# Optimization experiments

Measured on AMD Instinct MI355X. Metric: run time of the kernel, lower is better.

The kernel has to match this reference:

```python
import jax, jax.numpy as jnp
import numpy as np
import math

# dims: batch, seq_len, d_model, heads, head_dim
B, L, DM, H, DH = 1, 4096, 1024, 16, 64
BS, W, MAXD, DFF = 64, 16, 256, 4096  # block_size, band width (blocks), max rel distance, ffn dim
NB = L // BS


def _static_layout():
    # Static block-sparse causal band layout: tgt block n attends to src blocks [n-W+1 .. n].
    # Mirrors construct_blocksparse_rel_ids: rel = tgt_pos - src_pos, pos ids start at 1
    # (0 reserved for padding), clamp rel<-1 -> -1, rel>max_distance -> max_distance, then +1.
    n = np.arange(NB)[:, None, None, None]
    w = np.arange(W)[None, :, None, None]
    i = np.arange(BS)[None, None, :, None]
    j = np.arange(BS)[None, None, None, :]
    src_blk = n - (W - 1) + w
    # valid: block exists; diagonal block (w==W-1) is causal within-block (j<=i)
    valid = (src_blk >= 0) & ((w < W - 1) | (j <= i))
    tgt_pos = n * BS + i + 1
    src_pos = np.clip(src_blk, 0, None) * BS + j + 1
    rel = np.clip(tgt_pos - src_pos, -1, MAXD) + 1
    rel = np.where(valid, rel, 0)  # masked positions get rel id 0 (as in masked_fill_)
    src_idx = np.clip(np.arange(NB)[:, None] - (W - 1) + np.arange(W)[None, :], 0, None)
    return jnp.asarray(rel), jnp.asarray(valid), jnp.asarray(src_idx)

REL_IDS, VALID, SRC_IDX = _static_layout()  # [NB,W,BS,BS], [NB,W,BS,BS], [NB,W]


def _ln(x, g, b):
    m = x.mean(-1, keepdims=True)
    v = ((x - m) ** 2).mean(-1, keepdims=True)
    return (x - m) * jax.lax.rsqrt(v + 1e-5) * g + b


def setup_inputs() -> dict:
    key = jax.random.key(0)
    ks = jax.random.split(key, 10)
    p = lambda k, shape: jax.random.normal(k, shape, jnp.float32) * 0.02
    return dict(
        x=jax.random.normal(ks[0], (B, L, DM), jnp.float32),
        Wq=p(ks[1], (DM, DM)), Wk=p(ks[2], (DM, DM)), Wv=p(ks[3], (DM, DM)),
        Wo=p(ks[4], (DM, DM)),
        rel_emb=p(ks[5], (MAXD + 2, H)),  # per-head relative position bias table
        ln1_g=jnp.ones((DM,), jnp.float32), ln1_b=jnp.zeros((DM,), jnp.float32),
        ln2_g=jnp.ones((DM,), jnp.float32), ln2_b=jnp.zeros((DM,), jnp.float32),
        W1=p(ks[6], (DM, DFF)), b1=jnp.zeros((DFF,), jnp.float32),
        W2=p(ks[7], (DFF, DM)), b2=jnp.zeros((DM,), jnp.float32),
    )


def reference(x, Wq, Wk, Wv, Wo, rel_emb, ln1_g, ln1_b, ln2_g, ln2_b, W1, b1, W2, b2):
    h = _ln(x, ln1_g, ln1_b)

    def heads(Wt):
        return (h @ Wt).reshape(B, NB, BS, H, DH).transpose(0, 3, 1, 2, 4)  # [B,H,NB,BS,DH]

    q, k, v = heads(Wq), heads(Wk), heads(Wv)
    k_band = k[:, :, SRC_IDX]  # gather nonzero src blocks -> [B,H,NB,W,BS,DH]
    v_band = v[:, :, SRC_IDX]
    scores = jnp.einsum('bhnid,bhnwjd->bhniwj', q, k_band) / math.sqrt(DH)
    # relative position bias, per block pair and head
    bias = rel_emb[REL_IDS].transpose(4, 0, 2, 1, 3)  # [H,NB,BS,W,BS]
    scores = scores + bias[None]
    mask = VALID.transpose(0, 2, 1, 3)  # [NB,BS,W,BS]
    scores = jnp.where(mask, scores, jnp.float32(-1e30))
    p = jax.nn.softmax(scores.reshape(B, H, NB, BS, W * BS), axis=-1)
    p = p.reshape(B, H, NB, BS, W, BS)
    o = jnp.einsum('bhniwj,bhnwjd->bhnid', p, v_band)
    o = o.transpose(0, 2, 3, 1, 4).reshape(B, L, DM) @ Wo
    x = x + o
    h2 = _ln(x, ln2_g, ln2_b)
    x = x + (jax.nn.gelu(h2 @ W1 + b1) @ W2 + b2)
    return x
```

## Files before the change

kernel.cpp:

```cpp
#include <hip/hip_runtime.h>
#include <math.h>

typedef __bf16 bf16x8 __attribute__((ext_vector_type(8)));
typedef short  s16x4  __attribute__((ext_vector_type(4)));
typedef float  f32x4  __attribute__((ext_vector_type(4)));
typedef short  s16x8  __attribute__((ext_vector_type(8)));

__device__ __forceinline__ unsigned short f2bf(float f) {
    unsigned int u = __float_as_uint(f);
    u += 0x7fffu + ((u >> 16) & 1u);
    return (unsigned short)(u >> 16);
}

__device__ __forceinline__ unsigned cvt_pk_bf16(float a, float b) {
    unsigned r;
    asm volatile("v_cvt_pk_bf16_f32 %0, %1, %2" : "=v"(r) : "v"(a), "v"(b));
    return r;
}

__device__ __forceinline__ f32x4 mfma16(s16x4 a, s16x4 b, f32x4 c) {
#if __has_builtin(__builtin_amdgcn_mfma_f32_16x16x16bf16_1k)
    return __builtin_amdgcn_mfma_f32_16x16x16bf16_1k(a, b, c, 0, 0, 0);
#else
    asm volatile("s_nop 3\n\t"
                 "v_mfma_f32_16x16x16_bf16 %0, %1, %2, %0\n\t"
                 "s_nop 7\n\t"
                 "s_nop 7"
                 : "+v"(c) : "v"(a), "v"(b));
    return c;
#endif
}

__device__ __forceinline__ float gelu_tanh(float x) {
    float x3 = x * x * x;
    float t = tanhf(0.7978845608028654f * (x + 0.044715f * x3));
    return 0.5f * x * (1.0f + t);
}

__global__ __launch_bounds__(256) void tcvt_kernel(const float* __restrict__ in,
                                                   unsigned short* __restrict__ out,
                                                   int K, int N) {
    __shared__ float tile[32][33];
    int tx = threadIdx.x, ty = threadIdx.y;
    int k0 = blockIdx.y * 32, n0 = blockIdx.x * 32;
#pragma unroll
    for (int s = 0; s < 4; ++s)
        tile[ty + s * 8][tx] = in[(size_t)(k0 + ty + s * 8) * N + n0 + tx];
    __syncthreads();
#pragma unroll
    for (int s = 0; s < 4; ++s)
        out[(size_t)(n0 + ty + s * 8) * K + k0 + tx] = f2bf(tile[tx][ty + s * 8]);
}

__global__ __launch_bounds__(256) void ln_kernel(const float* __restrict__ x,
                                                 const float* __restrict__ g,
                                                 const float* __restrict__ b,
                                                 unsigned short* __restrict__ out) {
    int row = blockIdx.x;
    int tid = threadIdx.x;
    float4 v = ((const float4*)(x + (size_t)row * 1024))[tid];
    float s  = v.x + v.y + v.z + v.w;
    float ss = v.x * v.x + v.y * v.y + v.z * v.z + v.w * v.w;
#pragma unroll
    for (int o = 32; o > 0; o >>= 1) { s += __shfl_down(s, o); ss += __shfl_down(ss, o); }
    __shared__ float red[8];
    if ((tid & 63) == 0) { red[(tid >> 6) * 2] = s; red[(tid >> 6) * 2 + 1] = ss; }
    __syncthreads();
    s  = red[0] + red[2] + red[4] + red[6];
    ss = red[1] + red[3] + red[5] + red[7];
    float mean = s * (1.0f / 1024.0f);
    float var  = ss * (1.0f / 1024.0f) - mean * mean;
    float rs   = rsqrtf(var + 1e-5f);
    float4 gv = ((const float4*)g)[tid];
    float4 bv = ((const float4*)b)[tid];
    ushort4 o4;
    o4.x = f2bf((v.x - mean) * rs * gv.x + bv.x);
    o4.y = f2bf((v.y - mean) * rs * gv.y + bv.y);
    o4.z = f2bf((v.z - mean) * rs * gv.z + bv.z);
    o4.w = f2bf((v.w - mean) * rs * gv.w + bv.w);
    ((ushort4*)(out + (size_t)row * 1024))[tid] = o4;
}

__global__ __launch_bounds__(256) void tvt_kernel(const unsigned short* __restrict__ in,
                                                  unsigned short* __restrict__ out) {
    __shared__ unsigned short tile[64][72];
    int t = threadIdx.x;
    int l0 = blockIdx.x * 64, c0 = blockIdx.y * 64;
    int tr = t >> 3, tc = (t & 7) * 8;
#pragma unroll
    for (int s = 0; s < 2; ++s) {
        int r = tr + s * 32;
        s16x8 v = *(const s16x8*)(in + (size_t)(l0 + r) * 3072 + 2048 + c0 + tc);
        *(s16x8*)(&tile[r][tc]) = v;
    }
    __syncthreads();
#pragma unroll
    for (int s = 0; s < 2; ++s) {
        int c = tr + s * 32;
        s16x8 w;
#pragma unroll
        for (int e = 0; e < 8; ++e) w[e] = (short)tile[tc + e][c];
        *(s16x8*)(out + (size_t)(c0 + c) * 4096 + l0 + tc) = w;
    }
}

__device__ __forceinline__ void stage8(const unsigned short* __restrict__ src_row0, int ld,
                                       unsigned short* ldsdst, int lane) {
    const int r8 = lane >> 3;
    const int c  = (lane & 7) ^ r8;
    const unsigned short* src = src_row0 + (size_t)r8 * ld + c * 8;
    __builtin_amdgcn_global_load_lds((const __attribute__((address_space(1))) void*)src,
                                     (__attribute__((address_space(3))) void*)ldsdst, 16, 0, 0);
}

__device__ __forceinline__ void stage64(const unsigned short* __restrict__ mat, int ld,
                                        int grow0, int kcol,
                                        unsigned short* lds_tile, int q, int wave, int lane) {
    const int l8 = lane >> 3;
    const int sc = ((lane & 7) ^ l8) << 3;
    const unsigned short* src = mat + (size_t)(grow0 + q * 64 + wave * 8 + l8) * ld + kcol + sc;
    unsigned short* dst = lds_tile + ((q * 64 + wave * 8) << 6);
    __builtin_amdgcn_global_load_lds((const __attribute__((address_space(1))) void*)src,
                                     (__attribute__((address_space(3))) void*)dst, 16, 0, 0);
}

__device__ __forceinline__ bf16x8 ldfrag(const unsigned short* tile, int row, int chunk) {
    return *(const bf16x8*)(tile + (row << 6) + (((chunk ^ row) & 7) << 3));
}

__device__ __forceinline__ s16x4 ldfrag64(const unsigned short* tile, int row, int ch16, int half) {
    return *(const s16x4*)(tile + (row << 6) + (((ch16 ^ row) & 7) << 3) + (half << 2));
}

template <int EPI>
__global__ __launch_bounds__(512, 2) void gemm256_kernel(
        const unsigned short* __restrict__ A, int lda,
        const unsigned short* __restrict__ Bt, int ldb,
        void* __restrict__ Cv, const float* __restrict__ bias,
        int ldc, int NT, int gm, int gn, unsigned long long slab_stride) {
    extern __shared__ unsigned short lds[];
    unsigned short* sA = lds;
    unsigned short* sB = lds + 2 * 256 * 64;

    const int tid  = threadIdx.x;
    const int wave = tid >> 6, lane = tid & 63;
    const int wr = wave >> 2, wc = wave & 3;
    const int lg = lane >> 4, l15 = lane & 15;

    const int nwg = gridDim.x;
    const int bid = blockIdx.x;
    const int q8 = nwg >> 3, r8 = nwg & 7;
    const int xcd = bid & 7, loc = bid >> 3;
    const int swz = (xcd < r8 ? xcd * (q8 + 1) : r8 * (q8 + 1) + (xcd - r8) * q8) + loc;
    const int split = swz / (gm * gn);
    const int rem   = swz % (gm * gn);
    const int brow = (rem / gn) << 8;
    const int bcol = (rem % gn) << 8;
    const int kbase = split * (NT << 6);

    f32x4 acc[8][4] = {};

#define STAGE_A(tt, q_, pbuf) stage64(A, lda, brow, kbase + ((tt) << 6), sA + (pbuf) * 16384, (q_), wave, lane)
#define STAGE_B(tt, q_, pbuf) stage64(Bt, ldb, bcol, kbase + ((tt) << 6), sB + (pbuf) * 16384, (q_), wave, lane)

    STAGE_A(0, 0, 0); STAGE_A(0, 1, 0); STAGE_A(0, 2, 0); STAGE_A(0, 3, 0);
    STAGE_B(0, 0, 0); STAGE_B(0, 1, 0); STAGE_B(0, 2, 0); STAGE_B(0, 3, 0);
    STAGE_A(1, 0, 1); STAGE_A(1, 1, 1); STAGE_A(1, 2, 1); STAGE_A(1, 3, 1);
    STAGE_B(1, 0, 1); STAGE_B(1, 1, 1);
    asm volatile("s_waitcnt vmcnt(6)" ::: "memory");
    __builtin_amdgcn_s_barrier();

    for (int t = 0; t < NT; ++t) {
        const int p = t & 1;
        const unsigned short* tA = sA + p * 16384;
        const unsigned short* tB = sB + p * 16384;
        bf16x8 a0[4][2], a1[4][2], b0[2][2], b1[2][2];

#pragma unroll
        for (int im = 0; im < 4; ++im)
#pragma unroll
            for (int kk = 0; kk < 2; ++kk)
                a0[im][kk] = ldfrag(tA, wr * 128 + im * 16 + l15, lg + kk * 4);
#pragma unroll
        for (int in = 0; in < 2; ++in)
#pragma unroll
            for (int kk = 0; kk < 2; ++kk)
                b0[in][kk] = ldfrag(tB, wc * 64 + in * 16 + l15, lg + kk * 4);
        if (t + 1 < NT) { STAGE_B(t + 1, 2, p ^ 1); STAGE_B(t + 1, 3, p ^ 1); }
        __builtin_amdgcn_s_barrier();
        asm volatile("s_waitcnt lgkmcnt(0)" ::: "memory");
        __builtin_amdgcn_sched_barrier(0);
        __builtin_amdgcn_s_setprio(1);
#pragma unroll
        for (int kk = 0; kk < 2; ++kk)
#pragma unroll
            for (int im = 0; im < 4; ++im)
#pragma unroll
                for (int in = 0; in < 2; ++in)
                    acc[im][in] = __builtin_amdgcn_mfma_f32_16x16x32_bf16(a0[im][kk], b0[in][kk], acc[im][in], 0, 0, 0);
        __builtin_amdgcn_s_setprio(0);
        __builtin_amdgcn_s_barrier();

#pragma unroll
        for (int im = 0; im < 4; ++im)
#pragma unroll
            for (int kk = 0; kk < 2; ++kk)
                a1[im][kk] = ldfrag(tA, wr * 128 + 64 + im * 16 + l15, lg + kk * 4);
        if (t + 2 < NT) { STAGE_A(t + 2, 0, p); STAGE_A(t + 2, 2, p); }
        __builtin_amdgcn_s_barrier();
        asm volatile("s_waitcnt lgkmcnt(0)" ::: "memory");
        __builtin_amdgcn_sched_barrier(0);
        __builtin_amdgcn_s_setprio(1);
#pragma unroll
        for (int kk = 0; kk < 2; ++kk)
#pragma unroll
            for (int im = 0; im < 4; ++im)
#pragma unroll
                for (int in = 0; in < 2; ++in)
                    acc[4 + im][in] = __builtin_amdgcn_mfma_f32_16x16x32_bf16(a1[im][kk], b0[in][kk], acc[4 + im][in], 0, 0, 0);
        __builtin_amdgcn_s_setprio(0);
        __builtin_amdgcn_s_barrier();

#pragma unroll
        for (int in = 0; in < 2; ++in)
#pragma unroll
            for (int kk = 0; kk < 2; ++kk)
                b1[in][kk] = ldfrag(tB, wc * 64 + 32 + in * 16 + l15, lg + kk * 4);
        if (t + 2 < NT) { STAGE_A(t + 2, 1, p); STAGE_A(t + 2, 3, p); }
        __builtin_amdgcn_s_barrier();
        asm volatile("s_waitcnt lgkmcnt(0)" ::: "memory");
        __builtin_amdgcn_sched_barrier(0);
        __builtin_amdgcn_s_setprio(1);
#pragma unroll
        for (int kk = 0; kk < 2; ++kk)
#pragma unroll
            for (int im = 0; im < 4; ++im)
#pragma unroll
                for (int in = 0; in < 2; ++in)
                    acc[4 + im][2 + in] = __builtin_amdgcn_mfma_f32_16x16x32_bf16(a1[im][kk], b1[in][kk], acc[4 + im][2 + in], 0, 0, 0);
        __builtin_amdgcn_s_setprio(0);
        __builtin_amdgcn_s_barrier();

        if (t + 2 < NT) { STAGE_B(t + 2, 0, p); STAGE_B(t + 2, 1, p); }
        __builtin_amdgcn_s_barrier();
        asm volatile("s_waitcnt lgkmcnt(0)" ::: "memory");
        __builtin_amdgcn_sched_barrier(0);
        __builtin_amdgcn_s_setprio(1);
#pragma unroll
        for (int kk = 0; kk < 2; ++kk)
#pragma unroll
            for (int im = 0; im < 4; ++im)
#pragma unroll
                for (int in = 0; in < 2; ++in)
                    acc[im][2 + in] = __builtin_amdgcn_mfma_f32_16x16x32_bf16(a0[im][kk], b1[in][kk], acc[im][2 + in], 0, 0, 0);
        __builtin_amdgcn_s_setprio(0);
        if (t + 2 < NT) asm volatile("s_waitcnt vmcnt(6)" ::: "memory");
        else            asm volatile("s_waitcnt vmcnt(0)" ::: "memory");
        __builtin_amdgcn_s_barrier();
    }
#undef STAGE_A
#undef STAGE_B

#pragma unroll
    for (int mi = 0; mi < 8; ++mi)
#pragma unroll
        for (int ni = 0; ni < 4; ++ni)
#pragma unroll
            for (int rr = 0; rr < 4; ++rr) {
                int row = brow + wr * 128 + mi * 16 + lg * 4 + rr;
                int col = bcol + wc * 64 + ni * 16 + l15;
                float v = acc[mi][ni][rr];
                if (EPI == 0) {
                    ((unsigned short*)Cv)[(size_t)row * ldc + col] = f2bf(v);
                } else if (EPI == 2) {
                    v += bias[col];
                    ((unsigned short*)Cv)[(size_t)row * ldc + col] = f2bf(gelu_tanh(v));
                } else {
                    ((unsigned short*)Cv)[slab_stride * split + (size_t)row * ldc + col] = f2bf(v);
                }
            }
}

template <int HB>
__global__ __launch_bounds__(256) void reduce4_kernel(const unsigned short* __restrict__ part,
                                                      const float* __restrict__ bias,
                                                      const float* __restrict__ resid,
                                                      float* __restrict__ out) {
    int i4 = blockIdx.x * 256 + threadIdx.x;
    float4 r  = ((const float4*)resid)[i4];
    float s0 = r.x, s1 = r.y, s2 = r.z, s3 = r.w;
    if (HB) {
        float4 bb = ((const float4*)bias)[i4 & 255];
        s0 += bb.x; s1 += bb.y; s2 += bb.z; s3 += bb.w;
    }
#pragma unroll
    for (int s = 0; s < 4; ++s) {
        ushort4 u = ((const ushort4*)(part + (size_t)s * 4194304))[i4];
        s0 += __uint_as_float((unsigned)u.x << 16);
        s1 += __uint_as_float((unsigned)u.y << 16);
        s2 += __uint_as_float((unsigned)u.z << 16);
        s3 += __uint_as_float((unsigned)u.w << 16);
    }
    float4 o; o.x = s0; o.y = s1; o.z = s2; o.w = s3;
    ((float4*)out)[i4] = o;
}

__global__ __launch_bounds__(512, 4) void attn3_kernel(const unsigned short* __restrict__ qkv,
                                                       const unsigned short* __restrict__ vt,
                                                       const float* __restrict__ rel_emb,
                                                       unsigned short* __restrict__ outp) {
    const int lid   = blockIdx.y * gridDim.x + blockIdx.x;
    const int rid   = (lid & 7) * 64 + (lid >> 3);
    const int h     = rid >> 5;
    const int strip = rid & 31;
    const int n0    = strip * 2;

    const int tid  = threadIdx.x;
    const int wv   = tid >> 6;
    const int lane = tid & 63;
    const int qb   = wv >> 2;
    const int lg   = lane >> 4;
    const int l15  = lane & 15;
    const int iq   = (wv & 3) * 16 + l15;
    const int q0   = n0 * 64 + wv * 16;

    __shared__ __align__(16) unsigned short sK[2][4096];
    __shared__ __align__(16) unsigned short sV[2][4096];
    __shared__ float sRelF[258];

    bf16x8 qf[2];
    {
        const unsigned short* qrow = qkv + (size_t)(q0 + l15) * 3072 + h * 64 + lg * 8;
        qf[0] = *(const bf16x8*)(qrow);
        qf[1] = *(const bf16x8*)(qrow + 32);
    }

    for (int i = tid; i < 258; i += 512) sRelF[i] = rel_emb[i * 16 + h];
    const float relC = rel_emb[257 * 16 + h];

    const int tlo = (n0 >= 15) ? 0 : (15 - n0);
    {
        const int src = n0 - 15 + tlo;
        stage8(qkv + (size_t)(src * 64 + wv * 8) * 3072 + 1024 + h * 64, 3072, &sK[0][wv * 8 * 64], lane);
        stage8(vt + (size_t)(h * 64 + wv * 8) * 4096 + src * 64, 4096, &sV[0][wv * 8 * 64], lane);
    }
    asm volatile("s_waitcnt lgkmcnt(0)" ::: "memory");
    __builtin_amdgcn_s_barrier();

    f32x4 oacc[4] = {};
    float mrow = -3e38f, lrow = 0.f;

    for (int t = tlo; t <= 16; ++t) {
        const int cur = (t - tlo) & 1;
        if (t < 16) {
            const int src = n0 - 15 + (t + 1);
            stage8(qkv + (size_t)(src * 64 + wv * 8) * 3072 + 1024 + h * 64, 3072, &sK[cur ^ 1][wv * 8 * 64], lane);
            stage8(vt + (size_t)(h * 64 + wv * 8) * 4096 + src * 64, 4096, &sV[cur ^ 1][wv * 8 * 64], lane);
            asm volatile("s_waitcnt vmcnt(2)" ::: "memory");
        } else {
            asm volatile("s_waitcnt vmcnt(0)" ::: "memory");
        }
        __builtin_amdgcn_s_barrier();

        const bool act = (t >= qb) && (t - qb <= 15);
        if (act) {
            const unsigned short* tK = &sK[cur][0];
            const unsigned short* tV = &sV[cur][0];
            const int woff = 15 + qb - t;

            f32x4 st[4] = {};
            __builtin_amdgcn_s_setprio(1);
#pragma unroll
            for (int jt = 0; jt < 4; ++jt) {
                bf16x8 kf0 = ldfrag(tK, jt * 16 + l15, lg);
                bf16x8 kf1 = ldfrag(tK, jt * 16 + l15, lg + 4);
                st[jt] = __builtin_amdgcn_mfma_f32_16x16x32_bf16(kf0, qf[0], st[jt], 0, 0, 0);
                st[jt] = __builtin_amdgcn_mfma_f32_16x16x32_bf16(kf1, qf[1], st[jt], 0, 0, 0);
            }
            __builtin_amdgcn_s_setprio(0);

            float pm = -3e38f;
            if (woff >= 5) {
#pragma unroll
                for (int jt = 0; jt < 4; ++jt)
#pragma unroll
                    for (int rr = 0; rr < 4; ++rr) {
                        float v = st[jt][rr] * 0.125f + relC;
                        st[jt][rr] = v;
                        pm = fmaxf(pm, v);
                    }
            } else if (woff > 0) {
#pragma unroll
                for (int jt = 0; jt < 4; ++jt)
#pragma unroll
                    for (int rr = 0; rr < 4; ++rr) {
                        int j = jt * 16 + lg * 4 + rr;
                        int relid = min(woff * 64 + iq - j, 256) + 1;
                        float v = st[jt][rr] * 0.125f + sRelF[relid];
                        st[jt][rr] = v;
                        pm = fmaxf(pm, v);
                    }
            } else {
#pragma unroll
                for (int jt = 0; jt < 4; ++jt)
#pragma unroll
                    for (int rr = 0; rr < 4; ++rr) {
                        int j = jt * 16 + lg * 4 + rr;
                        float v = (j <= iq) ? (st[jt][rr] * 0.125f + sRelF[iq - j + 1]) : -1e30f;
                        st[jt][rr] = v;
                        pm = fmaxf(pm, v);
                    }
            }
            pm = fmaxf(pm, __shfl_xor(pm, 16));
            pm = fmaxf(pm, __shfl_xor(pm, 32));
            float mn  = fmaxf(mrow, pm);
            float scl = __expf(mrow - mn);
            mrow = mn;

            float rs = 0.f;
            unsigned pk0[4], pk1[4];
#pragma unroll
            for (int jt = 0; jt < 4; ++jt) {
                float p0 = __expf(st[jt][0] - mn);
                float p1 = __expf(st[jt][1] - mn);
                float p2 = __expf(st[jt][2] - mn);
                float p3 = __expf(st[jt][3] - mn);
                rs += (p0 + p1) + (p2 + p3);
                pk0[jt] = cvt_pk_bf16(p0, p1);
                pk1[jt] = cvt_pk_bf16(p2, p3);
            }
            rs += __shfl_xor(rs, 16);
            rs += __shfl_xor(rs, 32);
            lrow = lrow * scl + rs;
#pragma unroll
            for (int dt = 0; dt < 4; ++dt)
#pragma unroll
                for (int rr = 0; rr < 4; ++rr)
                    oacc[dt][rr] *= scl;

            __builtin_amdgcn_s_setprio(1);
#pragma unroll
            for (int ks = 0; ks < 4; ++ks) {
                union { unsigned u[2]; s16x4 v; } pu;
                pu.u[0] = pk0[ks]; pu.u[1] = pk1[ks];
#pragma unroll
                for (int dt = 0; dt < 4; ++dt) {
                    s16x4 vf = ldfrag64(tV, dt * 16 + l15, 2 * ks + (lg >> 1), lg & 1);
                    oacc[dt] = mfma16(vf, pu.v, oacc[dt]);
                }
            }
            __builtin_amdgcn_s_setprio(0);
        }
        __builtin_amdgcn_s_barrier();
    }

    float inv = 1.0f / lrow;
    unsigned short* sO = &sK[0][0] + wv * 1024;
#pragma unroll
    for (int dt = 0; dt < 4; ++dt)
#pragma unroll
        for (int c = 0; c < 2; ++c) {
            unsigned pr = cvt_pk_bf16(oacc[dt][2 * c] * inv, oacc[dt][2 * c + 1] * inv);
            int d  = dt * 16 + lg * 4 + 2 * c;
            int off = (l15 << 6) + ((((d >> 3) ^ (l15 & 7)) & 7) << 3) + (d & 7);
            *(unsigned*)(sO + off) = pr;
        }
#pragma unroll
    for (int c2 = 0; c2 < 2; ++c2) {
        int ch = lg + 4 * c2;
        bf16x8 ov = ldfrag(sO, l15, ch);
        *(s16x8*)(outp + (size_t)(q0 + l15) * 1024 + h * 64 + ch * 8) = *(const s16x8*)&ov;
    }
}

extern "C" void kernel_launch(void* const* d_in, const int* in_sizes, int n_in,
                              void* d_out, int out_size, void* d_ws, size_t ws_size,
                              hipStream_t stream) {
    const float* x    = (const float*)d_in[0];
    const float* Wq   = (const float*)d_in[1];
    const float* Wk   = (const float*)d_in[2];
    const float* Wv   = (const float*)d_in[3];
    const float* Wo   = (const float*)d_in[4];
    const float* rel  = (const float*)d_in[5];
    const float* ln1g = (const float*)d_in[6];
    const float* ln1b = (const float*)d_in[7];
    const float* ln2g = (const float*)d_in[8];
    const float* ln2b = (const float*)d_in[9];
    const float* W1   = (const float*)d_in[10];
    const float* b1   = (const float*)d_in[11];
    const float* W2   = (const float*)d_in[12];
    const float* b2   = (const float*)d_in[13];

    char* ws = (char*)d_ws;
    unsigned short* wqkvT  = (unsigned short*)(ws + 0);
    unsigned short* woT    = (unsigned short*)(ws + 6291456);
    unsigned short* attnb  = (unsigned short*)(ws + 8388608);
    unsigned short* w1T    = (unsigned short*)(ws + 16777216);
    unsigned short* hbuf   = (unsigned short*)(ws + 25165824);
    unsigned short* w2T    = (unsigned short*)(ws + 33554432);
    float*          x2     = (float*)(ws + 41943040);
    unsigned short* qkv    = (unsigned short*)(ws + 58720256);
    unsigned short* vt     = (unsigned short*)(ws + 83886080);
    unsigned short* wopart = (unsigned short*)(ws + 58720256);
    unsigned short* gbuf   = (unsigned short*)(ws + 58720256);
    unsigned short* part   = (unsigned short*)(ws + 0);

    const int smem = 131072;
    hipFuncSetAttribute((const void*)gemm256_kernel<0>, hipFuncAttributeMaxDynamicSharedMemorySize, smem);
    hipFuncSetAttribute((const void*)gemm256_kernel<2>, hipFuncAttributeMaxDynamicSharedMemorySize, smem);
    hipFuncSetAttribute((const void*)gemm256_kernel<4>, hipFuncAttributeMaxDynamicSharedMemorySize, smem);

    dim3 tb(32, 8);
    tcvt_kernel<<<dim3(32, 32), tb, 0, stream>>>(Wq, wqkvT, 1024, 1024);
    tcvt_kernel<<<dim3(32, 32), tb, 0, stream>>>(Wk, wqkvT + 1048576, 1024, 1024);
    tcvt_kernel<<<dim3(32, 32), tb, 0, stream>>>(Wv, wqkvT + 2097152, 1024, 1024);
    tcvt_kernel<<<dim3(32, 32), tb, 0, stream>>>(Wo, woT, 1024, 1024);
    tcvt_kernel<<<dim3(128, 32), tb, 0, stream>>>(W1, w1T, 1024, 4096);
    tcvt_kernel<<<dim3(32, 128), tb, 0, stream>>>(W2, w2T, 4096, 1024);

    ln_kernel<<<4096, 256, 0, stream>>>(x, ln1g, ln1b, hbuf);

    gemm256_kernel<0><<<192, 512, smem, stream>>>(hbuf, 1024, wqkvT, 1024, qkv,
                                                  nullptr, 3072, 16, 16, 12, 0ULL);

    tvt_kernel<<<dim3(64, 16), 256, 0, stream>>>(qkv, vt);

    attn3_kernel<<<dim3(32, 16), 512, 0, stream>>>(qkv, vt, rel, attnb);

    gemm256_kernel<4><<<256, 512, smem, stream>>>(attnb, 1024, woT, 1024, wopart,
                                                  nullptr, 1024, 4, 16, 4, 4194304ULL);
    reduce4_kernel<0><<<4096, 256, 0, stream>>>(wopart, nullptr, x, x2);

    ln_kernel<<<4096, 256, 0, stream>>>(x2, ln2g, ln2b, hbuf);

    gemm256_kernel<2><<<256, 512, smem, stream>>>(hbuf, 1024, w1T, 1024, gbuf,
                                                  b1, 4096, 16, 16, 16, 0ULL);

    gemm256_kernel<4><<<256, 512, smem, stream>>>(gbuf, 4096, w2T, 4096, part,
                                                  nullptr, 1024, 16, 16, 4, 4194304ULL);

    reduce4_kernel<1><<<4096, 256, 0, stream>>>(part, b2, x2, (float*)d_out);
}
```

Before: 246.6 us.

## Fuse reduce+LN2, batch weight converts, reshape attention blocks, band-swizzle GEMM tiles

Merges the Wo split-K reduction with the second layernorm so x2 is not re-read. Merges four weight transpose-convert launches into one 3D-grid launch. Restructures attention so each 256-thread block handles one query block instead of two, which removes the inactive-wave iterations of the paired-strip schedule. Remaps GEMM tile order into bands of four column tiles for better L2 reuse. The changes add more attention blocks with less K/V sharing per block.

```diff
diff --git a/kernel.cpp b/kernel.cpp
--- a/kernel.cpp
+++ b/kernel.cpp
@@ -35,6 +35,26 @@
     float x3 = x * x * x;
     float t = tanhf(0.7978845608028654f * (x + 0.044715f * x3));
     return 0.5f * x * (1.0f + t);
+}
+
+__global__ __launch_bounds__(256) void tcvt4_kernel(const float* __restrict__ p0,
+                                                    const float* __restrict__ p1,
+                                                    const float* __restrict__ p2,
+                                                    const float* __restrict__ p3,
+                                                    unsigned short* __restrict__ out) {
+    __shared__ float tile[32][33];
+    int z = blockIdx.z;
+    const float* in = (z == 0) ? p0 : (z == 1) ? p1 : (z == 2) ? p2 : p3;
+    unsigned short* o = out + (size_t)z * 1048576;
+    int tx = threadIdx.x, ty = threadIdx.y;
+    int k0 = blockIdx.y * 32, n0 = blockIdx.x * 32;
+#pragma unroll
+    for (int s = 0; s < 4; ++s)
+        tile[ty + s * 8][tx] = in[(size_t)(k0 + ty + s * 8) * 1024 + n0 + tx];
+    __syncthreads();
+#pragma unroll
+    for (int s = 0; s < 4; ++s)
+        o[(size_t)(n0 + ty + s * 8) * 1024 + k0 + tx] = f2bf(tile[tx][ty + s * 8]);
 }
 
 __global__ __launch_bounds__(256) void tcvt_kernel(const float* __restrict__ in,
@@ -81,6 +101,50 @@
     ((ushort4*)(out + (size_t)row * 1024))[tid] = o4;
 }
 
+__global__ __launch_bounds__(256) void reduceln_kernel(const unsigned short* __restrict__ part,
+                                                       const float* __restrict__ xin,
+                                                       const float* __restrict__ g,
+                                                       const float* __restrict__ b,
+                                                       float* __restrict__ x2,
+                                                       unsigned short* __restrict__ outbf) {
+    int row = blockIdx.x;
+    int tid = threadIdx.x;
+    int i4  = row * 256 + tid;
+    float4 r = ((const float4*)xin)[i4];
+    float v0 = r.x, v1 = r.y, v2 = r.z, v3 = r.w;
+#pragma unroll
+    for (int sl = 0; sl < 4; ++sl) {
+        ushort4 u = ((const ushort4*)(part + (size_t)sl * 4194304))[i4];
+        v0 += __uint_as_float((unsigned)u.x << 16);
+        v1 += __uint_as_float((unsigned)u.y << 16);
+        v2 += __uint_as_float((unsigned)u.z << 16);
+        v3 += __uint_as_float((unsigned)u.w << 16);
+    }
+    float4 o; o.x = v0; o.y = v1; o.z = v2; o.w = v3;
+    ((float4*)x2)[i4] = o;
+
+    float s  = v0 + v1 + v2 + v3;
+    float ss = v0 * v0 + v1 * v1 + v2 * v2 + v3 * v3;
+#pragma unroll
+    for (int off = 32; off > 0; off >>= 1) { s += __shfl_down(s, off); ss += __shfl_down(ss, off); }
+    __shared__ float red[8];
+    if ((tid & 63) == 0) { red[(tid >> 6) * 2] = s; red[(tid >> 6) * 2 + 1] = ss; }
+    __syncthreads();
+    s  = red[0] + red[2] + red[4] + red[6];
+    ss = red[1] + red[3] + red[5] + red[7];
+    float mean = s * (1.0f / 1024.0f);
+    float var  = ss * (1.0f / 1024.0f) - mean * mean;
+    float rs   = rsqrtf(var + 1e-5f);
+    float4 gv = ((const float4*)g)[tid];
+    float4 bv = ((const float4*)b)[tid];
+    ushort4 o4;
+    o4.x = f2bf((v0 - mean) * rs * gv.x + bv.x);
+    o4.y = f2bf((v1 - mean) * rs * gv.y + bv.y);
+    o4.z = f2bf((v2 - mean) * rs * gv.z + bv.z);
+    o4.w = f2bf((v3 - mean) * rs * gv.w + bv.w);
+    ((ushort4*)(outbf + (size_t)row * 1024))[tid] = o4;
+}
+
 __global__ __launch_bounds__(256) void tvt_kernel(const unsigned short* __restrict__ in,
                                                   unsigned short* __restrict__ out) {
     __shared__ unsigned short tile[64][72];
@@ -154,8 +218,10 @@
     const int swz = (xcd < r8 ? xcd * (q8 + 1) : r8 * (q8 + 1) + (xcd - r8) * q8) + loc;
     const int split = swz / (gm * gn);
     const int rem   = swz % (gm * gn);
-    const int brow = (rem / gn) << 8;
-    const int bcol = (rem % gn) << 8;
+    const int band = rem / (gm * 4);
+    const int r2   = rem % (gm * 4);
+    const int brow = (r2 >> 2) << 8;
+    const int bcol = (band * 4 + (r2 & 3)) << 8;
     const int kbase = split * (NT << 6);
 
     f32x4 acc[8][4] = {};
@@ -281,18 +347,14 @@
             }
 }
 
-template <int HB>
 __global__ __launch_bounds__(256) void reduce4_kernel(const unsigned short* __restrict__ part,
                                                       const float* __restrict__ bias,
                                                       const float* __restrict__ resid,
                                                       float* __restrict__ out) {
     int i4 = blockIdx.x * 256 + threadIdx.x;
     float4 r  = ((const float4*)resid)[i4];
-    float s0 = r.x, s1 = r.y, s2 = r.z, s3 = r.w;
-    if (HB) {
-        float4 bb = ((const float4*)bias)[i4 & 255];
-        s0 += bb.x; s1 += bb.y; s2 += bb.z; s3 += bb.w;
-    }
+    float4 bb = ((const float4*)bias)[i4 & 255];
+    float s0 = r.x + bb.x, s1 = r.y + bb.y, s2 = r.z + bb.z, s3 = r.w + bb.w;
 #pragma unroll
     for (int s = 0; s < 4; ++s) {
         ushort4 u = ((const ushort4*)(part + (size_t)s * 4194304))[i4];
@@ -305,24 +367,22 @@
     ((float4*)out)[i4] = o;
 }
 
-__global__ __launch_bounds__(512, 4) void attn3_kernel(const unsigned short* __restrict__ qkv,
+__global__ __launch_bounds__(256, 4) void attn4_kernel(const unsigned short* __restrict__ qkv,
                                                        const unsigned short* __restrict__ vt,
                                                        const float* __restrict__ rel_emb,
                                                        unsigned short* __restrict__ outp) {
-    const int lid   = blockIdx.y * gridDim.x + blockIdx.x;
-    const int rid   = (lid & 7) * 64 + (lid >> 3);
-    const int h     = rid >> 5;
-    const int strip = rid & 31;
-    const int n0    = strip * 2;
+    const int lid = blockIdx.y * gridDim.x + blockIdx.x;
+    const int rid = (lid & 7) * 128 + (lid >> 3);
+    const int h   = rid >> 6;
+    const int n   = rid & 63;
 
     const int tid  = threadIdx.x;
     const int wv   = tid >> 6;
     const int lane = tid & 63;
-    const int qb   = wv >> 2;
     const int lg   = lane >> 4;
     const int l15  = lane & 15;
-    const int iq   = (wv & 3) * 16 + l15;
-    const int q0   = n0 * 64 + wv * 16;
+    const int iq   = wv * 16 + l15;
+    const int q0   = n * 64 + wv * 16;
 
     __shared__ __align__(16) unsigned short sK[2][4096];
     __shared__ __align__(16) unsigned short sV[2][4096];
@@ -335,14 +395,18 @@
         qf[1] = *(const bf16x8*)(qrow + 32);
     }
 
-    for (int i = tid; i < 258; i += 512) sRelF[i] = rel_emb[i * 16 + h];
+    for (int i = tid; i < 258; i += 256) sRelF[i] = rel_emb[i * 16 + h];
     const float relC = rel_emb[257 * 16 + h];
 
-    const int tlo = (n0 >= 15) ? 0 : (15 - n0);
+    const int tlo = (n >= 15) ? 0 : (15 - n);
     {
-        const int src = n0 - 15 + tlo;
-        stage8(qkv + (size_t)(src * 64 + wv * 8) * 3072 + 1024 + h * 64, 3072, &sK[0][wv * 8 * 64], lane);
-        stage8(vt + (size_t)(h * 64 + wv * 8) * 4096 + src * 64, 4096, &sV[0][wv * 8 * 64], lane);
+        const int src = n - 15 + tlo;
+#pragma unroll
+        for (int s = 0; s < 2; ++s) {
+            int r0 = wv * 16 + s * 8;
+            stage8(qkv + (size_t)(src * 64 + r0) * 3072 + 1024 + h * 64, 3072, &sK[0][r0 * 64], lane);
+            stage8(vt + (size_t)(h * 64 + r0) * 4096 + src * 64, 4096, &sV[0][r0 * 64], lane);
+        }
     }
     asm volatile("s_waitcnt lgkmcnt(0)" ::: "memory");
     __builtin_amdgcn_s_barrier();
@@ -350,107 +414,108 @@
     f32x4 oacc[4] = {};
     float mrow = -3e38f, lrow = 0.f;
 
-    for (int t = tlo; t <= 16; ++t) {
+    for (int t = tlo; t < 16; ++t) {
         const int cur = (t - tlo) & 1;
-        if (t < 16) {
-            const int src = n0 - 15 + (t + 1);
-            stage8(qkv + (size_t)(src * 64 + wv * 8) * 3072 + 1024 + h * 64, 3072, &sK[cur ^ 1][wv * 8 * 64], lane);
-            stage8(vt + (size_t)(h * 64 + wv * 8) * 4096 + src * 64, 4096, &sV[cur ^ 1][wv * 8 * 64], lane);
-            asm volatile("s_waitcnt vmcnt(2)" ::: "memory");
+        if (t < 15) {
+            const int src = n - 15 + (t + 1);
+#pragma unroll
+            for (int s = 0; s < 2; ++s) {
+                int r0 = wv * 16 + s * 8;
+                stage8(qkv + (size_t)(src * 64 + r0) * 3072 + 1024 + h * 64, 3072, &sK[cur ^ 1][r0 * 64], lane);
+                stage8(vt + (size_t)(h * 64 + r0) * 4096 + src * 64, 4096, &sV[cur ^ 1][r0 * 64], lane);
+            }
+            asm volatile("s_waitcnt vmcnt(4)" ::: "memory");
         } else {
             asm volatile("s_waitcnt vmcnt(0)" ::: "memory");
         }
         __builtin_amdgcn_s_barrier();
 
-        const bool act = (t >= qb) && (t - qb <= 15);
-        if (act) {
-            const unsigned short* tK = &sK[cur][0];
-            const unsigned short* tV = &sV[cur][0];
-            const int woff = 15 + qb - t;
-
-            f32x4 st[4] = {};
-            __builtin_amdgcn_s_setprio(1);
-#pragma unroll
-            for (int jt = 0; jt < 4; ++jt) {
-                bf16x8 kf0 = ldfrag(tK, jt * 16 + l15, lg);
-                bf16x8 kf1 = ldfrag(tK, jt * 16 + l15, lg + 4);
-                st[jt] = __builtin_amdgcn_mfma_f32_16x16x32_bf16(kf0, qf[0], st[jt], 0, 0, 0);
-                st[jt] = __builtin_amdgcn_mfma_f32_16x16x32_bf16(kf1, qf[1], st[jt], 0, 0, 0);
+        const unsigned short* tK = &sK[cur][0];
+        const unsigned short* tV = &sV[cur][0];
+        const int woff = 15 - t;
+
+        f32x4 st[4] = {};
+        __builtin_amdgcn_s_setprio(1);
+#pragma unroll
+        for (int jt = 0; jt < 4; ++jt) {
+            bf16x8 kf0 = ldfrag(tK, jt * 16 + l15, lg);
+            bf16x8 kf1 = ldfrag(tK, jt * 16 + l15, lg + 4);
+            st[jt] = __builtin_amdgcn_mfma_f32_16x16x32_bf16(kf0, qf[0], st[jt], 0, 0, 0);
+            st[jt] = __builtin_amdgcn_mfma_f32_16x16x32_bf16(kf1, qf[1], st[jt], 0, 0, 0);
+        }
+        __builtin_amdgcn_s_setprio(0);
+
+        float pm = -3e38f;
+        if (woff >= 5) {
+#pragma unroll
+            for (int jt = 0; jt < 4; ++jt)
+#pragma unroll
+                for (int rr = 0; rr < 4; ++rr) {
+                    float v = st[jt][rr] * 0.125f + relC;
+                    st[jt][rr] = v;
+                    pm = fmaxf(pm, v);
+                }
+        } else if (woff > 0) {
+#pragma unroll
+            for (int jt = 0; jt < 4; ++jt)
+#pragma unroll
+                for (int rr = 0; rr < 4; ++rr) {
+                    int j = jt * 16 + lg * 4 + rr;
+                    int relid = min(woff * 64 + iq - j, 256) + 1;
+                    float v = st[jt][rr] * 0.125f + sRelF[relid];
+                    st[jt][rr] = v;
+                    pm = fmaxf(pm, v);
+                }
+        } else {
+#pragma unroll
+            for (int jt = 0; jt < 4; ++jt)
+#pragma unroll
+                for (int rr = 0; rr < 4; ++rr) {
+                    int j = jt * 16 + lg * 4 + rr;
+                    float v = (j <= iq) ? (st[jt][rr] * 0.125f + sRelF[iq - j + 1]) : -1e30f;
+                    st[jt][rr] = v;
+                    pm = fmaxf(pm, v);
+                }
+        }
+        pm = fmaxf(pm, __shfl_xor(pm, 16));
+        pm = fmaxf(pm, __shfl_xor(pm, 32));
+        float mn  = fmaxf(mrow, pm);
+        float scl = __expf(mrow - mn);
+        mrow = mn;
+
+        float rs = 0.f;
+        unsigned pk0[4], pk1[4];
+#pragma unroll
+        for (int jt = 0; jt < 4; ++jt) {
+            float p0 = __expf(st[jt][0] - mn);
+            float p1 = __expf(st[jt][1] - mn);
+            float p2 = __expf(st[jt][2] - mn);
+            float p3 = __expf(st[jt][3] - mn);
+            rs += (p0 + p1) + (p2 + p3);
+            pk0[jt] = cvt_pk_bf16(p0, p1);
+            pk1[jt] = cvt_pk_bf16(p2, p3);
+        }
+        rs += __shfl_xor(rs, 16);
+        rs += __shfl_xor(rs, 32);
+        lrow = lrow * scl + rs;
+#pragma unroll
+        for (int dt = 0; dt < 4; ++dt)
+#pragma unroll
+            for (int rr = 0; rr < 4; ++rr)
+                oacc[dt][rr] *= scl;
+
+        __builtin_amdgcn_s_setprio(1);
+#pragma unroll
+        for (int ks = 0; ks < 4; ++ks) {
+            union { unsigned u[2]; s16x4 v; } pu;
+            pu.u[0] = pk0[ks]; pu.u[1] = pk1[ks];
+#pragma unroll
+            for (int dt = 0; dt < 4; ++dt) {
+                s16x4 vf = ldfrag64(tV, dt * 16 + l15, 2 * ks + (lg >> 1), lg & 1);
+                oacc[dt] = mfma16(vf, pu.v, oacc[dt]);
             }
-            __builtin_amdgcn_s_setprio(0);
-
-            float pm = -3e38f;
-            if (woff >= 5) {
-#pragma unroll
-                for (int jt = 0; jt < 4; ++jt)
-#pragma unroll
-                    for (int rr = 0; rr < 4; ++rr) {
-                        float v = st[jt][rr] * 0.125f + relC;
-                        st[jt][rr] = v;
-                        pm = fmaxf(pm, v);
-                    }
-            } else if (woff > 0) {
-#pragma unroll
-                for (int jt = 0; jt < 4; ++jt)
-#pragma unroll
-                    for (int rr = 0; rr < 4; ++rr) {
-                        int j = jt * 16 + lg * 4 + rr;
-                        int relid = min(woff * 64 + iq - j, 256) + 1;
-                        float v = st[jt][rr] * 0.125f + sRelF[relid];
-                        st[jt][rr] = v;
-                        pm = fmaxf(pm, v);
-                    }
-            } else {
-#pragma unroll
-                for (int jt = 0; jt < 4; ++jt)
-#pragma unroll
-                    for (int rr = 0; rr < 4; ++rr) {
-                        int j = jt * 16 + lg * 4 + rr;
-                        float v = (j <= iq) ? (st[jt][rr] * 0.125f + sRelF[iq - j + 1]) : -1e30f;
-                        st[jt][rr] = v;
-                        pm = fmaxf(pm, v);
-                    }
-            }
-            pm = fmaxf(pm, __shfl_xor(pm, 16));
-            pm = fmaxf(pm, __shfl_xor(pm, 32));
-            float mn  = fmaxf(mrow, pm);
-            float scl = __expf(mrow - mn);
-            mrow = mn;
-
-            float rs = 0.f;
-            unsigned pk0[4], pk1[4];
-#pragma unroll
-            for (int jt = 0; jt < 4; ++jt) {
-                float p0 = __expf(st[jt][0] - mn);
-                float p1 = __expf(st[jt][1] - mn);
-                float p2 = __expf(st[jt][2] - mn);
-                float p3 = __expf(st[jt][3] - mn);
-                rs += (p0 + p1) + (p2 + p3);
-                pk0[jt] = cvt_pk_bf16(p0, p1);
-                pk1[jt] = cvt_pk_bf16(p2, p3);
-            }
-            rs += __shfl_xor(rs, 16);
-            rs += __shfl_xor(rs, 32);
-            lrow = lrow * scl + rs;
-#pragma unroll
-            for (int dt = 0; dt < 4; ++dt)
-#pragma unroll
-                for (int rr = 0; rr < 4; ++rr)
-                    oacc[dt][rr] *= scl;
-
-            __builtin_amdgcn_s_setprio(1);
-#pragma unroll
-            for (int ks = 0; ks < 4; ++ks) {
-                union { unsigned u[2]; s16x4 v; } pu;
-                pu.u[0] = pk0[ks]; pu.u[1] = pk1[ks];
-#pragma unroll
-                for (int dt = 0; dt < 4; ++dt) {
-                    s16x4 vf = ldfrag64(tV, dt * 16 + l15, 2 * ks + (lg >> 1), lg & 1);
-                    oacc[dt] = mfma16(vf, pu.v, oacc[dt]);
-                }
-            }
-            __builtin_amdgcn_s_setprio(0);
         }
+        __builtin_amdgcn_s_setprio(0);
         __builtin_amdgcn_s_barrier();
     }
 
@@ -493,7 +558,7 @@
 
     char* ws = (char*)d_ws;
     unsigned short* wqkvT  = (unsigned short*)(ws + 0);
-    unsigned short* woT    = (unsigned short*)(ws + 6291456);
+    unsigned short* woT    = wqkvT + 3145728;
     unsigned short* attnb  = (unsigned short*)(ws + 8388608);
     unsigned short* w1T    = (unsigned short*)(ws + 16777216);
     unsigned short* hbuf   = (unsigned short*)(ws + 25165824);
@@ -511,10 +576,7 @@
     hipFuncSetAttribute((const void*)gemm256_kernel<4>, hipFuncAttributeMaxDynamicSharedMemorySize, smem);
 
     dim3 tb(32, 8);
-    tcvt_kernel<<<dim3(32, 32), tb, 0, stream>>>(Wq, wqkvT, 1024, 1024);
-    tcvt_kernel<<<dim3(32, 32), tb, 0, stream>>>(Wk, wqkvT + 1048576, 1024, 1024);
-    tcvt_kernel<<<dim3(32, 32), tb, 0, stream>>>(Wv, wqkvT + 2097152, 1024, 1024);
-    tcvt_kernel<<<dim3(32, 32), tb, 0, stream>>>(Wo, woT, 1024, 1024);
+    tcvt4_kernel<<<dim3(32, 32, 4), tb, 0, stream>>>(Wq, Wk, Wv, Wo, wqkvT);
     tcvt_kernel<<<dim3(128, 32), tb, 0, stream>>>(W1, w1T, 1024, 4096);
     tcvt_kernel<<<dim3(32, 128), tb, 0, stream>>>(W2, w2T, 4096, 1024);
 
@@ -525,13 +587,11 @@
 
     tvt_kernel<<<dim3(64, 16), 256, 0, stream>>>(qkv, vt);
 
-    attn3_kernel<<<dim3(32, 16), 512, 0, stream>>>(qkv, vt, rel, attnb);
+    attn4_kernel<<<dim3(64, 16), 256, 0, stream>>>(qkv, vt, rel, attnb);
 
     gemm256_kernel<4><<<256, 512, smem, stream>>>(attnb, 1024, woT, 1024, wopart,
                                                   nullptr, 1024, 4, 16, 4, 4194304ULL);
-    reduce4_kernel<0><<<4096, 256, 0, stream>>>(wopart, nullptr, x, x2);
-
-    ln_kernel<<<4096, 256, 0, stream>>>(x2, ln2g, ln2b, hbuf);
+    reduceln_kernel<<<4096, 256, 0, stream>>>(wopart, x, ln2g, ln2b, x2, hbuf);
 
     gemm256_kernel<2><<<256, 512, smem, stream>>>(hbuf, 1024, w1T, 1024, gbuf,
                                                   b1, 4096, 16, 16, 16, 0ULL);
@@ -539,5 +599,5 @@
     gemm256_kernel<4><<<256, 512, smem, stream>>>(gbuf, 4096, w2T, 4096, part,
                                                   nullptr, 1024, 16, 16, 4, 4194304ULL);
 
-    reduce4_kernel<1><<<4096, 256, 0, stream>>>(part, b2, x2, (float*)d_out);
-}
+    reduce4_kernel<<<4096, 256, 0, stream>>>(part, b2, x2, (float*)d_out);
+}
```

Measured after the change: 235.7 us. -4.4%, faster.
